# Kernel optimization log

Hardware: AMD Instinct MI355X
Metric: run time of the kernel (lower is better)

The kernel has to match this reference:

```python
import jax, jax.numpy as jnp
import numpy as np

BS, N, D, B, D_PM = 8, 4096, 1024, 8, 64
BUDGET = 16.0


def setup_inputs() -> dict:
    key = jax.random.key(0)
    ks = jax.random.split(key, 6)
    H = jax.random.normal(ks[0], (BS, N, D), jnp.float32)
    surprise = jax.random.normal(ks[1], (BS, N, D), jnp.float32)
    # W_pm initialized as (1/B)*I + small noise, as in initialize()
    eye = jnp.eye(D_PM, dtype=jnp.float32)
    W_pm = eye / B + 0.01 * jax.random.normal(ks[2], (BS, B, D_PM, D_PM), jnp.float32)
    proj_in_w = jax.random.normal(ks[3], (D_PM, D), jnp.float32) / np.float32(np.sqrt(D))
    proj_in_b = jnp.zeros((D_PM,), jnp.float32)
    # original zero-inits proj_out; use small values so output is non-trivial
    proj_out_w = 0.02 * jax.random.normal(ks[4], (D, D_PM), jnp.float32)
    proj_out_b = jnp.zeros((D,), jnp.float32)
    raw_beta = jnp.full((B,), -3.0, jnp.float32)
    raw_decay = jnp.full((B,), np.float32(np.log(0.999 / 0.001)), jnp.float32)  # logit(0.999)
    surp_scale = jnp.ones((1,), jnp.float32)
    surp_bias = jnp.zeros((1,), jnp.float32)
    return dict(H=H, surprise=surprise, W_pm=W_pm,
                proj_in_w=proj_in_w, proj_in_b=proj_in_b,
                proj_out_w=proj_out_w, proj_out_b=proj_out_b,
                raw_beta=raw_beta, raw_decay=raw_decay,
                surp_scale=surp_scale, surp_bias=surp_bias)


def reference(H, surprise, W_pm, proj_in_w, proj_in_b, proj_out_w, proj_out_b,
              raw_beta, raw_decay, surp_scale, surp_bias):
    # ---- read ----
    pre = jnp.einsum('bnd,pd->bnp', H, proj_in_w) + proj_in_b          # [BS,N,D_pm]
    W_sum = jnp.sum(W_pm, axis=1)                                      # [BS,D_pm,D_pm]
    post = jnp.einsum('bnp,bqp->bnq', pre, W_sum)                      # pre @ W_sum^T
    pm_read = jnp.einsum('bnq,dq->bnd', post, proj_out_w) + proj_out_b # [BS,N,D]
    # ---- commit (Hebbian, surprise-gated) ----
    surp_mag = jnp.linalg.norm(surprise, axis=-1)                      # [BS,N]
    s = jax.nn.sigmoid(surp_scale * surp_mag + surp_bias)              # [BS,N]
    weighted = jnp.sqrt(s)[..., None] * pre                            # [BS,N,D_pm]
    G = jnp.einsum('bnp,bnq->bpq', weighted, weighted) / N             # [BS,D_pm,D_pm]
    beta = jax.nn.softplus(raw_beta)                                   # [B]
    decay = jax.nn.sigmoid(raw_decay)                                  # [B]
    eye = jnp.eye(D_PM, dtype=pre.dtype)
    T = decay[None, :, None, None] * eye + beta[None, :, None, None] * G[:, None]  # [BS,B,D_pm,D_pm]
    W_new = jnp.einsum('bkij,bkjq->bkiq', W_pm, T)                     # [BS,B,D_pm,D_pm]
    frob = jnp.sqrt(jnp.sum(W_new * W_new, axis=(-2, -1), keepdims=True))
    scale = jnp.minimum(BUDGET / jnp.maximum(frob, 1e-8), 1.0)
    W_new = W_new * scale
    return pm_read, W_new
```

## Files before the change

kernel.cpp:

```cpp
#include <hip/hip_runtime.h>

typedef unsigned short u16;
typedef __attribute__((ext_vector_type(4))) float f32x4;
typedef __attribute__((ext_vector_type(8))) short s16x8;

static constexpr int N_ = 4096;
static constexpr int D_ = 1024;

__device__ __forceinline__ u16 f2bf(float f) {
  unsigned u = __float_as_uint(f);
  u += 0x7FFFu + ((u >> 16) & 1u);
  return (u16)(u >> 16);
}

__device__ __forceinline__ f32x4 zero4() {
  f32x4 z; z[0] = 0.f; z[1] = 0.f; z[2] = 0.f; z[3] = 0.f; return z;
}

__global__ __launch_bounds__(256) void k_prep(
    const float* __restrict__ Wpm, const float* __restrict__ piw,
    const float* __restrict__ pw, u16* __restrict__ WpB,
    u16* __restrict__ MB) {
  int bid = blockIdx.x, tid = threadIdx.x;
  if (bid < 16) {
    size_t i0 = (size_t)bid * 4096;
    for (int idx = tid; idx < 4096; idx += 256)
      WpB[i0 + idx] = f2bf(piw[i0 + idx]);
    return;
  }
  __shared__ float Ws[64][65];
  int idx2 = bid - 16;
  int b = idx2 >> 4, t = idx2 & 15;
  for (int idx = tid; idx < 4096; idx += 256) {
    float s = 0.f;
#pragma unroll
    for (int k = 0; k < 8; ++k)
      s += Wpm[((size_t)(b * 8 + k)) * 4096 + idx];
    Ws[idx >> 6][idx & 63] = s;
  }
  __syncthreads();
  u16* mb = MB + ((size_t)b << 16);
  for (int oidx = tid; oidx < 4096; oidx += 256) {
    int r = oidx >> 6, c = oidx & 63;
    int drow = t * 64 + r;
    const float* prow = pw + (size_t)drow * 64;
    float acc = 0.f;
#pragma unroll 8
    for (int q = 0; q < 64; ++q) acc += prow[q] * Ws[q][c];
    mb[(size_t)drow * 64 + c] = f2bf(acc);
  }
}

__global__ __launch_bounds__(512, 4) void k_main(
    const float* __restrict__ H, const float* __restrict__ Sur,
    const float* __restrict__ pib, const float* __restrict__ pob,
    const float* __restrict__ sscale_p, const float* __restrict__ sbias_p,
    const u16* __restrict__ WpB, const u16* __restrict__ MB,
    float* __restrict__ Gacc, float* __restrict__ out) {
  __shared__ float preF[64][68];
  __shared__ u16 preRP[64][72];
  __shared__ u16 wRP[64][72];
  __shared__ float sqs[64];

  const int tid = threadIdx.x;
  const int lane = tid & 63;
  const int w = tid >> 6;
  const int wm = w & 3;
  const int wk = w >> 2;
  const int llo = lane & 15;
  const int lhi = lane >> 4;
  const int b = blockIdx.x >> 6;
  const int row0 = (blockIdx.x & 63) * 64;

  {
    int r = w * 8 + (lane >> 3);
    const float* p = Sur + ((size_t)b * N_ + row0 + r) * D_ + (lane & 7) * 4;
    float a0 = 0.f, a1 = 0.f;
#pragma unroll 8
    for (int j = 0; j < 32; j += 2) {
      float4 v = *(const float4*)(p + j * 32);
      float4 v2 = *(const float4*)(p + j * 32 + 32);
      a0 += v.x * v.x + v.y * v.y + v.z * v.z + v.w * v.w;
      a1 += v2.x * v2.x + v2.y * v2.y + v2.z * v2.z + v2.w * v2.w;
    }
    float a = a0 + a1;
    a += __shfl_xor(a, 1, 64);
    a += __shfl_xor(a, 2, 64);
    a += __shfl_xor(a, 4, 64);
    if ((lane & 7) == 0) {
      float mag = sqrtf(a);
      float s = 1.f / (1.f + __expf(-(sscale_p[0] * mag + sbias_p[0])));
      sqs[r] = sqrtf(s);
    }
  }

  f32x4 accA[4];
#pragma unroll
  for (int t = 0; t < 4; ++t) accA[t] = zero4();
  {
    const float* hrow =
        H + ((size_t)b * N_ + row0 + wm * 16 + llo) * D_ + wk * 512 + lhi * 8;
    const u16* wp0 = WpB + (size_t)llo * 1024 + wk * 512 + lhi * 8;
#pragma unroll 2
    for (int k0 = 0; k0 < 512; k0 += 32) {
      float4 a0 = *(const float4*)(hrow + k0);
      float4 a1 = *(const float4*)(hrow + k0 + 4);
      s16x8 af;
      af[0] = (short)f2bf(a0.x); af[1] = (short)f2bf(a0.y);
      af[2] = (short)f2bf(a0.z); af[3] = (short)f2bf(a0.w);
      af[4] = (short)f2bf(a1.x); af[5] = (short)f2bf(a1.y);
      af[6] = (short)f2bf(a1.z); af[7] = (short)f2bf(a1.w);
#pragma unroll
      for (int t = 0; t < 4; ++t) {
        s16x8 bf = *(const s16x8*)(wp0 + (size_t)t * 16 * 1024 + k0);
        accA[t] = __builtin_amdgcn_mfma_f32_16x16x32_bf16(af, bf, accA[t], 0, 0, 0);
      }
    }
  }
  if (wk == 1) {
#pragma unroll
    for (int t = 0; t < 4; ++t)
#pragma unroll
      for (int r = 0; r < 4; ++r)
        preF[wm * 16 + lhi * 4 + r][t * 16 + llo] = accA[t][r];
  }
  __syncthreads();
  if (wk == 0) {
#pragma unroll
    for (int t = 0; t < 4; ++t) {
      float bias = pib[t * 16 + llo];
#pragma unroll
      for (int r = 0; r < 4; ++r) {
        int row = wm * 16 + lhi * 4 + r;
        float v = accA[t][r] + preF[row][t * 16 + llo] + bias;
        preRP[row][t * 16 + llo] = f2bf(v);
        wRP[row][t * 16 + llo] = f2bf(v * sqs[row]);
      }
    }
  }
  __syncthreads();

  {
    f32x4 accG[4];
#pragma unroll
    for (int t = 0; t < 4; ++t) accG[t] = zero4();
    int kbase = wk * 32;
    s16x8 ag;
#pragma unroll
    for (int j = 0; j < 8; ++j)
      ag[j] = (short)wRP[kbase + lhi * 8 + j][wm * 16 + llo];
#pragma unroll
    for (int t = 0; t < 4; ++t) {
      s16x8 bg;
#pragma unroll
      for (int j = 0; j < 8; ++j)
        bg[j] = (short)wRP[kbase + lhi * 8 + j][t * 16 + llo];
      accG[t] = __builtin_amdgcn_mfma_f32_16x16x32_bf16(ag, bg, accG[t], 0, 0, 0);
    }
    float* gb = Gacc + (size_t)b * 4096;
#pragma unroll
    for (int t = 0; t < 4; ++t)
#pragma unroll
      for (int r = 0; r < 4; ++r)
        atomicAdd(gb + (wm * 16 + lhi * 4 + r) * 64 + t * 16 + llo, accG[t][r]);
  }

  {
    s16x8 ad0 = *(const s16x8*)&preRP[wm * 16 + llo][lhi * 8];
    s16x8 ad1 = *(const s16x8*)&preRP[wm * 16 + llo][32 + lhi * 8];
    const u16* mb = MB + ((size_t)b << 16);
    float* orow = out + ((size_t)b * N_ + row0 + wm * 16) * D_;
    int nend = wk * 512 + 512;
    for (int n0 = wk * 512; n0 < nend; n0 += 16) {
      s16x8 b0 = *(const s16x8*)(mb + (size_t)(n0 + llo) * 64 + lhi * 8);
      s16x8 b1 = *(const s16x8*)(mb + (size_t)(n0 + llo) * 64 + 32 + lhi * 8);
      f32x4 acc = zero4();
      acc = __builtin_amdgcn_mfma_f32_16x16x32_bf16(ad0, b0, acc, 0, 0, 0);
      acc = __builtin_amdgcn_mfma_f32_16x16x32_bf16(ad1, b1, acc, 0, 0, 0);
      float bias = pob[n0 + llo];
#pragma unroll
      for (int r = 0; r < 4; ++r)
        orow[(size_t)(lhi * 4 + r) * D_ + n0 + llo] = acc[r] + bias;
    }
  }
}

__global__ __launch_bounds__(256) void k_wnew(
    const float* __restrict__ Wpm, const float* __restrict__ Gacc,
    const float* __restrict__ rbeta, const float* __restrict__ rdecay,
    float* __restrict__ outW) {
  __shared__ float Wk[64][66];
  __shared__ float Gl[64][66];
  __shared__ float red[4];
  int bk = blockIdx.x;
  int b = bk >> 3, k = bk & 7;
  int tid = threadIdx.x;
  const float* wsrc = Wpm + (size_t)bk * 4096;
  const float* gsrc = Gacc + (size_t)b * 4096;
  for (int idx = tid; idx < 4096; idx += 256) {
    Wk[idx >> 6][idx & 63] = wsrc[idx];
    Gl[idx >> 6][idx & 63] = gsrc[idx];
  }
  __syncthreads();
  float beta = log1pf(__expf(rbeta[k]));
  float decay = 1.f / (1.f + __expf(-rdecay[k]));
  float bn = beta * (1.f / 4096.f);
  int q = tid & 63;
  int rbase = tid >> 6;
  float vals[16];
  float ss = 0.f;
#pragma unroll
  for (int i = 0; i < 16; ++i) {
    int row = i * 4 + rbase;
    float acc = 0.f;
#pragma unroll 8
    for (int j = 0; j < 64; ++j) acc += Wk[row][j] * Gl[j][q];
    float v = decay * Wk[row][q] + bn * acc;
    vals[i] = v;
    ss += v * v;
  }
#pragma unroll
  for (int m = 1; m < 64; m <<= 1) ss += __shfl_xor(ss, m, 64);
  if ((tid & 63) == 0) red[tid >> 6] = ss;
  __syncthreads();
  float frob = sqrtf(red[0] + red[1] + red[2] + red[3]);
  float scale = fminf(16.f / fmaxf(frob, 1e-8f), 1.f);
  float* dst = outW + (size_t)bk * 4096;
#pragma unroll
  for (int i = 0; i < 16; ++i) dst[i * 256 + tid] = vals[i] * scale;
}

extern "C" void kernel_launch(void* const* d_in, const int* in_sizes, int n_in,
                              void* d_out, int out_size, void* d_ws, size_t ws_size,
                              hipStream_t stream) {
  const float* H      = (const float*)d_in[0];
  const float* Sur    = (const float*)d_in[1];
  const float* Wpm    = (const float*)d_in[2];
  const float* piw    = (const float*)d_in[3];
  const float* pib    = (const float*)d_in[4];
  const float* pw     = (const float*)d_in[5];
  const float* pob    = (const float*)d_in[6];
  const float* rbeta  = (const float*)d_in[7];
  const float* rdecay = (const float*)d_in[8];
  const float* sscale = (const float*)d_in[9];
  const float* sbias  = (const float*)d_in[10];
  float* out = (float*)d_out;

  char* ws = (char*)d_ws;
  float* Gacc = (float*)(ws);
  u16* WpB    = (u16*)(ws + 131072);
  u16* MB     = (u16*)(ws + 262144);

  hipMemsetAsync(Gacc, 0, 131072, stream);
  k_prep<<<144, 256, 0, stream>>>(Wpm, piw, pw, WpB, MB);
  k_main<<<512, 512, 0, stream>>>(H, Sur, pib, pob, sscale, sbias,
                                  WpB, MB, Gacc, out);
  k_wnew<<<64, 256, 0, stream>>>(Wpm, Gacc, rbeta, rdecay,
                                 out + (size_t)8 * 4096 * 1024);
}
```

Baseline: 165.6 us.

## Prefetch H and MB loads in registers, transpose wRP, fold Gacc zeroing

Software-pipelines the H loads in the projection GEMM with a 4-deep register buffer, and the MB loads in the output GEMM with a 2-deep buffer, so global latency overlaps with MFMA work. The weighted-pre tile is stored transposed in shared memory, so the Gram MFMA operands become single vector LDS reads instead of eight scalar gathers. Zeroing of the G accumulator moves into the prep kernel, which removes a separate memset launch. The cost is higher register pressure, which may reduce occupancy under the 512-thread launch bound.

```diff
diff --git a/kernel.cpp b/kernel.cpp
--- a/kernel.cpp
+++ b/kernel.cpp
@@ -20,12 +20,14 @@
 __global__ __launch_bounds__(256) void k_prep(
     const float* __restrict__ Wpm, const float* __restrict__ piw,
     const float* __restrict__ pw, u16* __restrict__ WpB,
-    u16* __restrict__ MB) {
+    u16* __restrict__ MB, float* __restrict__ Gacc) {
   int bid = blockIdx.x, tid = threadIdx.x;
   if (bid < 16) {
     size_t i0 = (size_t)bid * 4096;
     for (int idx = tid; idx < 4096; idx += 256)
       WpB[i0 + idx] = f2bf(piw[i0 + idx]);
+    float* g = Gacc + (size_t)bid * 2048;
+    for (int idx = tid; idx < 2048; idx += 256) g[idx] = 0.f;
     return;
   }
   __shared__ float Ws[64][65];
@@ -57,9 +59,9 @@
     const float* __restrict__ sscale_p, const float* __restrict__ sbias_p,
     const u16* __restrict__ WpB, const u16* __restrict__ MB,
     float* __restrict__ Gacc, float* __restrict__ out) {
-  __shared__ float preF[64][68];
-  __shared__ u16 preRP[64][72];
-  __shared__ u16 wRP[64][72];
+  __shared__ __align__(16) float preF[64][68];
+  __shared__ __align__(16) u16 preRP[64][72];
+  __shared__ __align__(16) u16 wRPT[64][72];
   __shared__ float sqs[64];
 
   const int tid = threadIdx.x;
@@ -76,7 +78,7 @@
     int r = w * 8 + (lane >> 3);
     const float* p = Sur + ((size_t)b * N_ + row0 + r) * D_ + (lane & 7) * 4;
     float a0 = 0.f, a1 = 0.f;
-#pragma unroll 8
+#pragma unroll
     for (int j = 0; j < 32; j += 2) {
       float4 v = *(const float4*)(p + j * 32);
       float4 v2 = *(const float4*)(p + j * 32 + 32);
@@ -101,19 +103,32 @@
     const float* hrow =
         H + ((size_t)b * N_ + row0 + wm * 16 + llo) * D_ + wk * 512 + lhi * 8;
     const u16* wp0 = WpB + (size_t)llo * 1024 + wk * 512 + lhi * 8;
-#pragma unroll 2
-    for (int k0 = 0; k0 < 512; k0 += 32) {
-      float4 a0 = *(const float4*)(hrow + k0);
-      float4 a1 = *(const float4*)(hrow + k0 + 4);
-      s16x8 af;
-      af[0] = (short)f2bf(a0.x); af[1] = (short)f2bf(a0.y);
-      af[2] = (short)f2bf(a0.z); af[3] = (short)f2bf(a0.w);
-      af[4] = (short)f2bf(a1.x); af[5] = (short)f2bf(a1.y);
-      af[6] = (short)f2bf(a1.z); af[7] = (short)f2bf(a1.w);
-#pragma unroll
-      for (int t = 0; t < 4; ++t) {
-        s16x8 bf = *(const s16x8*)(wp0 + (size_t)t * 16 * 1024 + k0);
-        accA[t] = __builtin_amdgcn_mfma_f32_16x16x32_bf16(af, bf, accA[t], 0, 0, 0);
+    float4 A0[4], A1[4];
+#pragma unroll
+    for (int i = 0; i < 4; ++i) {
+      A0[i] = *(const float4*)(hrow + i * 32);
+      A1[i] = *(const float4*)(hrow + i * 32 + 4);
+    }
+#pragma unroll
+    for (int kb = 0; kb < 512; kb += 128) {
+#pragma unroll
+      for (int jj = 0; jj < 4; ++jj) {
+        const int k0 = kb + jj * 32;
+        float4 a0 = A0[jj], a1 = A1[jj];
+        if (k0 + 128 < 512) {
+          A0[jj] = *(const float4*)(hrow + k0 + 128);
+          A1[jj] = *(const float4*)(hrow + k0 + 132);
+        }
+        s16x8 af;
+        af[0] = (short)f2bf(a0.x); af[1] = (short)f2bf(a0.y);
+        af[2] = (short)f2bf(a0.z); af[3] = (short)f2bf(a0.w);
+        af[4] = (short)f2bf(a1.x); af[5] = (short)f2bf(a1.y);
+        af[6] = (short)f2bf(a1.z); af[7] = (short)f2bf(a1.w);
+#pragma unroll
+        for (int t = 0; t < 4; ++t) {
+          s16x8 bf = *(const s16x8*)(wp0 + (size_t)t * 16384 + k0);
+          accA[t] = __builtin_amdgcn_mfma_f32_16x16x32_bf16(af, bf, accA[t], 0, 0, 0);
+        }
       }
     }
   }
@@ -134,27 +149,21 @@
         int row = wm * 16 + lhi * 4 + r;
         float v = accA[t][r] + preF[row][t * 16 + llo] + bias;
         preRP[row][t * 16 + llo] = f2bf(v);
-        wRP[row][t * 16 + llo] = f2bf(v * sqs[row]);
+        wRPT[t * 16 + llo][row] = f2bf(v * sqs[row]);
       }
     }
   }
   __syncthreads();
 
   {
+    const int kbase = wk * 32;
     f32x4 accG[4];
 #pragma unroll
     for (int t = 0; t < 4; ++t) accG[t] = zero4();
-    int kbase = wk * 32;
-    s16x8 ag;
-#pragma unroll
-    for (int j = 0; j < 8; ++j)
-      ag[j] = (short)wRP[kbase + lhi * 8 + j][wm * 16 + llo];
+    s16x8 ag = *(const s16x8*)&wRPT[wm * 16 + llo][kbase + lhi * 8];
 #pragma unroll
     for (int t = 0; t < 4; ++t) {
-      s16x8 bg;
-#pragma unroll
-      for (int j = 0; j < 8; ++j)
-        bg[j] = (short)wRP[kbase + lhi * 8 + j][t * 16 + llo];
+      s16x8 bg = *(const s16x8*)&wRPT[t * 16 + llo][kbase + lhi * 8];
       accG[t] = __builtin_amdgcn_mfma_f32_16x16x32_bf16(ag, bg, accG[t], 0, 0, 0);
     }
     float* gb = Gacc + (size_t)b * 4096;
@@ -169,14 +178,25 @@
     s16x8 ad0 = *(const s16x8*)&preRP[wm * 16 + llo][lhi * 8];
     s16x8 ad1 = *(const s16x8*)&preRP[wm * 16 + llo][32 + lhi * 8];
     const u16* mb = MB + ((size_t)b << 16);
+    const int nb = wk * 512;
+    const u16* mrow0 = mb + (size_t)(nb + llo) * 64 + lhi * 8;
     float* orow = out + ((size_t)b * N_ + row0 + wm * 16) * D_;
-    int nend = wk * 512 + 512;
-    for (int n0 = wk * 512; n0 < nend; n0 += 16) {
-      s16x8 b0 = *(const s16x8*)(mb + (size_t)(n0 + llo) * 64 + lhi * 8);
-      s16x8 b1 = *(const s16x8*)(mb + (size_t)(n0 + llo) * 64 + 32 + lhi * 8);
+    s16x8 B0[2], B1[2];
+    B0[0] = *(const s16x8*)(mrow0);
+    B1[0] = *(const s16x8*)(mrow0 + 32);
+    B0[1] = *(const s16x8*)(mrow0 + 1024);
+    B1[1] = *(const s16x8*)(mrow0 + 1024 + 32);
+#pragma unroll 2
+    for (int i = 0; i < 32; ++i) {
+      const int j = i & 1;
+      s16x8 b0 = B0[j], b1 = B1[j];
+      int ipf = (i + 2 < 32) ? (i + 2) : i;
+      B0[j] = *(const s16x8*)(mrow0 + (size_t)ipf * 1024);
+      B1[j] = *(const s16x8*)(mrow0 + (size_t)ipf * 1024 + 32);
       f32x4 acc = zero4();
       acc = __builtin_amdgcn_mfma_f32_16x16x32_bf16(ad0, b0, acc, 0, 0, 0);
       acc = __builtin_amdgcn_mfma_f32_16x16x32_bf16(ad1, b1, acc, 0, 0, 0);
+      const int n0 = nb + i * 16;
       float bias = pob[n0 + llo];
 #pragma unroll
       for (int r = 0; r < 4; ++r)
@@ -251,8 +271,7 @@
   u16* WpB    = (u16*)(ws + 131072);
   u16* MB     = (u16*)(ws + 262144);
 
-  hipMemsetAsync(Gacc, 0, 131072, stream);
-  k_prep<<<144, 256, 0, stream>>>(Wpm, piw, pw, WpB, MB);
+  k_prep<<<144, 256, 0, stream>>>(Wpm, piw, pw, WpB, MB, Gacc);
   k_main<<<512, 512, 0, stream>>>(H, Sur, pib, pob, sscale, sbias,
                                   WpB, MB, Gacc, out);
   k_wnew<<<64, 256, 0, stream>>>(Wpm, Gacc, rbeta, rdecay,
```

Result: no change. 168.1 us (+1.5%).

## Split fused main kernel into projection, read/Gram, and Gram-reduce stages

Applied to the files above, without the earlier changes.

Splits the single fused kernel into three. k1 uses small 16-row blocks: it computes the surprise gates and the input projection with a split-K over 4 waves, batching loads up front. k23 sums the four bf16 partial projections, builds the Gram tile and the output read with vectorized float4 stores. Per-block Gram partials are written in bf16 and reduced by k_gred, replacing the global float atomics and the memset. This adds bf16 round-trips through global memory for the projection partials and Gram partials, which costs extra traffic, two more launches and some precision.

```diff
diff --git a/kernel.cpp b/kernel.cpp
--- a/kernel.cpp
+++ b/kernel.cpp
@@ -1,26 +1,33 @@
 #include <hip/hip_runtime.h>
 
 typedef unsigned short u16;
+typedef unsigned int u32;
 typedef __attribute__((ext_vector_type(4))) float f32x4;
 typedef __attribute__((ext_vector_type(8))) short s16x8;
+typedef __attribute__((ext_vector_type(4))) short s16x4;
 
 static constexpr int N_ = 4096;
 static constexpr int D_ = 1024;
+
+#define MEMCLOB() asm volatile("" ::: "memory")
 
 __device__ __forceinline__ u16 f2bf(float f) {
   unsigned u = __float_as_uint(f);
   u += 0x7FFFu + ((u >> 16) & 1u);
   return (u16)(u >> 16);
 }
-
+__device__ __forceinline__ float bf2f(u16 v) {
+  return __uint_as_float((u32)v << 16);
+}
 __device__ __forceinline__ f32x4 zero4() {
   f32x4 z; z[0] = 0.f; z[1] = 0.f; z[2] = 0.f; z[3] = 0.f; return z;
 }
 
-__global__ __launch_bounds__(256) void k_prep(
+__global__ __launch_bounds__(256) void k_aux(
     const float* __restrict__ Wpm, const float* __restrict__ piw,
     const float* __restrict__ pw, u16* __restrict__ WpB,
     u16* __restrict__ MB) {
+  __shared__ float Ws[64][65];
   int bid = blockIdx.x, tid = threadIdx.x;
   if (bid < 16) {
     size_t i0 = (size_t)bid * 4096;
@@ -28,7 +35,6 @@
       WpB[i0 + idx] = f2bf(piw[i0 + idx]);
     return;
   }
-  __shared__ float Ws[64][65];
   int idx2 = bid - 16;
   int b = idx2 >> 4, t = idx2 & 15;
   for (int idx = tid; idx < 4096; idx += 256) {
@@ -51,17 +57,85 @@
   }
 }
 
-__global__ __launch_bounds__(512, 4) void k_main(
+__global__ __launch_bounds__(256, 4) void k1(
     const float* __restrict__ H, const float* __restrict__ Sur,
-    const float* __restrict__ pib, const float* __restrict__ pob,
     const float* __restrict__ sscale_p, const float* __restrict__ sbias_p,
-    const u16* __restrict__ WpB, const u16* __restrict__ MB,
-    float* __restrict__ Gacc, float* __restrict__ out) {
-  __shared__ float preF[64][68];
-  __shared__ u16 preRP[64][72];
-  __shared__ u16 wRP[64][72];
-  __shared__ float sqs[64];
-
+    const u16* __restrict__ WpB, u16* __restrict__ preQ,
+    float* __restrict__ sqs_ws) {
+  const int tid = threadIdx.x;
+  const int lane = tid & 63;
+  const int w = tid >> 6;
+  const int llo = lane & 15;
+  const int lhi = lane >> 4;
+  const int b = blockIdx.x >> 8;
+  const int row0 = (blockIdx.x & 255) * 16;
+
+  {
+    const float* sp =
+        Sur + ((size_t)b * N_ + row0 + (tid >> 4)) * D_ + (tid & 15) * 4;
+    float4 sv[16];
+#pragma unroll
+    for (int i = 0; i < 16; ++i) sv[i] = *(const float4*)(sp + i * 64);
+    MEMCLOB();
+    float a = 0.f;
+#pragma unroll
+    for (int i = 0; i < 16; ++i)
+      a += sv[i].x * sv[i].x + sv[i].y * sv[i].y + sv[i].z * sv[i].z +
+           sv[i].w * sv[i].w;
+    a += __shfl_xor(a, 1, 64);
+    a += __shfl_xor(a, 2, 64);
+    a += __shfl_xor(a, 4, 64);
+    a += __shfl_xor(a, 8, 64);
+    if ((tid & 15) == 0) {
+      float mag = sqrtf(a);
+      float s = 1.f / (1.f + __expf(-(sscale_p[0] * mag + sbias_p[0])));
+      sqs_ws[b * N_ + row0 + (tid >> 4)] = sqrtf(s);
+    }
+  }
+
+  const float* hrow =
+      H + ((size_t)b * N_ + row0 + llo) * D_ + w * 256 + lhi * 8;
+  float4 ah[16];
+#pragma unroll
+  for (int c = 0; c < 8; ++c) {
+    ah[2 * c] = *(const float4*)(hrow + c * 32);
+    ah[2 * c + 1] = *(const float4*)(hrow + c * 32 + 4);
+  }
+  MEMCLOB();
+  f32x4 acc[4];
+#pragma unroll
+  for (int t = 0; t < 4; ++t) acc[t] = zero4();
+  const u16* wpb = WpB + w * 256 + lhi * 8;
+#pragma unroll
+  for (int c = 0; c < 8; ++c) {
+    s16x8 af;
+    af[0] = (short)f2bf(ah[2 * c].x); af[1] = (short)f2bf(ah[2 * c].y);
+    af[2] = (short)f2bf(ah[2 * c].z); af[3] = (short)f2bf(ah[2 * c].w);
+    af[4] = (short)f2bf(ah[2 * c + 1].x); af[5] = (short)f2bf(ah[2 * c + 1].y);
+    af[6] = (short)f2bf(ah[2 * c + 1].z); af[7] = (short)f2bf(ah[2 * c + 1].w);
+#pragma unroll
+    for (int t = 0; t < 4; ++t) {
+      s16x8 bs = *(const s16x8*)(wpb + (size_t)(t * 16 + llo) * 1024 + c * 32);
+      acc[t] = __builtin_amdgcn_mfma_f32_16x16x32_bf16(bs, af, acc[t], 0, 0, 0);
+    }
+  }
+  u16* pq = preQ + ((size_t)w << 21) + ((size_t)(b * N_ + row0 + llo)) * 64;
+#pragma unroll
+  for (int t = 0; t < 4; ++t) {
+    s16x4 v;
+#pragma unroll
+    for (int r = 0; r < 4; ++r) v[r] = (short)f2bf(acc[t][r]);
+    *(s16x4*)(pq + t * 16 + lhi * 4) = v;
+  }
+}
+
+__global__ __launch_bounds__(512, 4) void k23(
+    const u16* __restrict__ preQ, const float* __restrict__ pib,
+    const float* __restrict__ pob, const u16* __restrict__ MB,
+    const float* __restrict__ sqs_ws, u16* __restrict__ GpartB,
+    float* __restrict__ out) {
+  __shared__ __align__(16) u16 preRP[64 * 80];
+  __shared__ __align__(16) u16 wRPT[64 * 80];
   const int tid = threadIdx.x;
   const int lane = tid & 63;
   const int w = tid >> 6;
@@ -73,120 +147,97 @@
   const int row0 = (blockIdx.x & 63) * 64;
 
   {
-    int r = w * 8 + (lane >> 3);
-    const float* p = Sur + ((size_t)b * N_ + row0 + r) * D_ + (lane & 7) * 4;
-    float a0 = 0.f, a1 = 0.f;
+    const int row = tid >> 3, col0 = (tid & 7) * 8;
+    const u16* pq = preQ + ((size_t)(b * N_ + row0 + row)) * 64 + col0;
+    float sum[8] = {0, 0, 0, 0, 0, 0, 0, 0};
+#pragma unroll
+    for (int q = 0; q < 4; ++q) {
+      s16x8 v = *(const s16x8*)(pq + (size_t)q * 2097152);
+#pragma unroll
+      for (int j = 0; j < 8; ++j) sum[j] += bf2f((u16)v[j]);
+    }
+    float4 bb0 = *(const float4*)&pib[col0];
+    float4 bb1 = *(const float4*)&pib[col0 + 4];
+    sum[0] += bb0.x; sum[1] += bb0.y; sum[2] += bb0.z; sum[3] += bb0.w;
+    sum[4] += bb1.x; sum[5] += bb1.y; sum[6] += bb1.z; sum[7] += bb1.w;
+    float sq = sqs_ws[b * N_ + row0 + row];
+    s16x8 pr;
+#pragma unroll
+    for (int j = 0; j < 8; ++j) pr[j] = (short)f2bf(sum[j]);
+    *(s16x8*)&preRP[row * 80 + col0] = pr;
+#pragma unroll
+    for (int j = 0; j < 8; ++j)
+      wRPT[(col0 + j) * 80 + row] = f2bf(sum[j] * sq);
+  }
+  __syncthreads();
+
+  {
+    s16x8 ag = *(const s16x8*)&wRPT[(wm * 16 + llo) * 80 + wk * 32 + lhi * 8];
+    f32x4 accG[4];
+#pragma unroll
+    for (int t = 0; t < 4; ++t) {
+      s16x8 bg = *(const s16x8*)&wRPT[(t * 16 + llo) * 80 + wk * 32 + lhi * 8];
+      accG[t] = __builtin_amdgcn_mfma_f32_16x16x32_bf16(ag, bg, zero4(), 0, 0, 0);
+    }
+    u16* gout = GpartB + ((size_t)blockIdx.x * 2 + wk) * 4096;
+#pragma unroll
+    for (int t = 0; t < 4; ++t)
+#pragma unroll
+      for (int r = 0; r < 4; ++r)
+        gout[(wm * 16 + lhi * 4 + r) * 64 + t * 16 + llo] = f2bf(accG[t][r]);
+  }
+
+  {
+    s16x8 ad0 = *(const s16x8*)&preRP[(wm * 16 + llo) * 80 + lhi * 8];
+    s16x8 ad1 = *(const s16x8*)&preRP[(wm * 16 + llo) * 80 + 32 + lhi * 8];
+    const u16* mcol = MB + ((size_t)b << 16) + (size_t)(wk * 512) * 64 + lhi * 8;
+    float* orow = out + ((size_t)b * N_ + row0 + wm * 16 + llo) * D_ + wk * 512;
+    const float* pobw = pob + wk * 512;
+#pragma unroll
+    for (int c = 0; c < 8; ++c) {
+      s16x8 f0[4], f1[4];
+#pragma unroll
+      for (int i = 0; i < 4; ++i) {
+        const u16* p = mcol + (size_t)(c * 64 + i * 16 + llo) * 64;
+        f0[i] = *(const s16x8*)p;
+        f1[i] = *(const s16x8*)(p + 32);
+      }
+#pragma unroll
+      for (int i = 0; i < 4; ++i) {
+        f32x4 acc = zero4();
+        acc = __builtin_amdgcn_mfma_f32_16x16x32_bf16(f0[i], ad0, acc, 0, 0, 0);
+        acc = __builtin_amdgcn_mfma_f32_16x16x32_bf16(f1[i], ad1, acc, 0, 0, 0);
+        int n0 = c * 64 + i * 16 + lhi * 4;
+        float4 bias4 = *(const float4*)&pobw[n0];
+        float4 o;
+        o.x = acc[0] + bias4.x;
+        o.y = acc[1] + bias4.y;
+        o.z = acc[2] + bias4.z;
+        o.w = acc[3] + bias4.w;
+        *(float4*)(orow + n0) = o;
+      }
+    }
+  }
+}
+
+__global__ __launch_bounds__(256) void k_gred(
+    const u16* __restrict__ GpartB, float* __restrict__ Gsum) {
+  __shared__ float red[4][64];
+  int b = blockIdx.x >> 6, g = blockIdx.x & 63;
+  int lane = threadIdx.x & 63, q = threadIdx.x >> 6;
+  const u16* src = GpartB + ((size_t)(b * 128 + q * 32)) * 4096 + g * 64 + lane;
+  float s = 0.f;
 #pragma unroll 8
-    for (int j = 0; j < 32; j += 2) {
-      float4 v = *(const float4*)(p + j * 32);
-      float4 v2 = *(const float4*)(p + j * 32 + 32);
-      a0 += v.x * v.x + v.y * v.y + v.z * v.z + v.w * v.w;
-      a1 += v2.x * v2.x + v2.y * v2.y + v2.z * v2.z + v2.w * v2.w;
-    }
-    float a = a0 + a1;
-    a += __shfl_xor(a, 1, 64);
-    a += __shfl_xor(a, 2, 64);
-    a += __shfl_xor(a, 4, 64);
-    if ((lane & 7) == 0) {
-      float mag = sqrtf(a);
-      float s = 1.f / (1.f + __expf(-(sscale_p[0] * mag + sbias_p[0])));
-      sqs[r] = sqrtf(s);
-    }
-  }
-
-  f32x4 accA[4];
-#pragma unroll
-  for (int t = 0; t < 4; ++t) accA[t] = zero4();
-  {
-    const float* hrow =
-        H + ((size_t)b * N_ + row0 + wm * 16 + llo) * D_ + wk * 512 + lhi * 8;
-    const u16* wp0 = WpB + (size_t)llo * 1024 + wk * 512 + lhi * 8;
-#pragma unroll 2
-    for (int k0 = 0; k0 < 512; k0 += 32) {
-      float4 a0 = *(const float4*)(hrow + k0);
-      float4 a1 = *(const float4*)(hrow + k0 + 4);
-      s16x8 af;
-      af[0] = (short)f2bf(a0.x); af[1] = (short)f2bf(a0.y);
-      af[2] = (short)f2bf(a0.z); af[3] = (short)f2bf(a0.w);
-      af[4] = (short)f2bf(a1.x); af[5] = (short)f2bf(a1.y);
-      af[6] = (short)f2bf(a1.z); af[7] = (short)f2bf(a1.w);
-#pragma unroll
-      for (int t = 0; t < 4; ++t) {
-        s16x8 bf = *(const s16x8*)(wp0 + (size_t)t * 16 * 1024 + k0);
-        accA[t] = __builtin_amdgcn_mfma_f32_16x16x32_bf16(af, bf, accA[t], 0, 0, 0);
-      }
-    }
-  }
-  if (wk == 1) {
-#pragma unroll
-    for (int t = 0; t < 4; ++t)
-#pragma unroll
-      for (int r = 0; r < 4; ++r)
-        preF[wm * 16 + lhi * 4 + r][t * 16 + llo] = accA[t][r];
-  }
-  __syncthreads();
-  if (wk == 0) {
-#pragma unroll
-    for (int t = 0; t < 4; ++t) {
-      float bias = pib[t * 16 + llo];
-#pragma unroll
-      for (int r = 0; r < 4; ++r) {
-        int row = wm * 16 + lhi * 4 + r;
-        float v = accA[t][r] + preF[row][t * 16 + llo] + bias;
-        preRP[row][t * 16 + llo] = f2bf(v);
-        wRP[row][t * 16 + llo] = f2bf(v * sqs[row]);
-      }
-    }
-  }
-  __syncthreads();
-
-  {
-    f32x4 accG[4];
-#pragma unroll
-    for (int t = 0; t < 4; ++t) accG[t] = zero4();
-    int kbase = wk * 32;
-    s16x8 ag;
-#pragma unroll
-    for (int j = 0; j < 8; ++j)
-      ag[j] = (short)wRP[kbase + lhi * 8 + j][wm * 16 + llo];
-#pragma unroll
-    for (int t = 0; t < 4; ++t) {
-      s16x8 bg;
-#pragma unroll
-      for (int j = 0; j < 8; ++j)
-        bg[j] = (short)wRP[kbase + lhi * 8 + j][t * 16 + llo];
-      accG[t] = __builtin_amdgcn_mfma_f32_16x16x32_bf16(ag, bg, accG[t], 0, 0, 0);
-    }
-    float* gb = Gacc + (size_t)b * 4096;
-#pragma unroll
-    for (int t = 0; t < 4; ++t)
-#pragma unroll
-      for (int r = 0; r < 4; ++r)
-        atomicAdd(gb + (wm * 16 + lhi * 4 + r) * 64 + t * 16 + llo, accG[t][r]);
-  }
-
-  {
-    s16x8 ad0 = *(const s16x8*)&preRP[wm * 16 + llo][lhi * 8];
-    s16x8 ad1 = *(const s16x8*)&preRP[wm * 16 + llo][32 + lhi * 8];
-    const u16* mb = MB + ((size_t)b << 16);
-    float* orow = out + ((size_t)b * N_ + row0 + wm * 16) * D_;
-    int nend = wk * 512 + 512;
-    for (int n0 = wk * 512; n0 < nend; n0 += 16) {
-      s16x8 b0 = *(const s16x8*)(mb + (size_t)(n0 + llo) * 64 + lhi * 8);
-      s16x8 b1 = *(const s16x8*)(mb + (size_t)(n0 + llo) * 64 + 32 + lhi * 8);
-      f32x4 acc = zero4();
-      acc = __builtin_amdgcn_mfma_f32_16x16x32_bf16(ad0, b0, acc, 0, 0, 0);
-      acc = __builtin_amdgcn_mfma_f32_16x16x32_bf16(ad1, b1, acc, 0, 0, 0);
-      float bias = pob[n0 + llo];
-#pragma unroll
-      for (int r = 0; r < 4; ++r)
-        orow[(size_t)(lhi * 4 + r) * D_ + n0 + llo] = acc[r] + bias;
-    }
-  }
+  for (int i = 0; i < 32; ++i) s += bf2f(src[(size_t)i * 4096]);
+  red[q][lane] = s;
+  __syncthreads();
+  if (q == 0)
+    Gsum[(size_t)b * 4096 + g * 64 + lane] =
+        red[0][lane] + red[1][lane] + red[2][lane] + red[3][lane];
 }
 
 __global__ __launch_bounds__(256) void k_wnew(
-    const float* __restrict__ Wpm, const float* __restrict__ Gacc,
+    const float* __restrict__ Wpm, const float* __restrict__ Gsum,
     const float* __restrict__ rbeta, const float* __restrict__ rdecay,
     float* __restrict__ outW) {
   __shared__ float Wk[64][66];
@@ -196,7 +247,7 @@
   int b = bk >> 3, k = bk & 7;
   int tid = threadIdx.x;
   const float* wsrc = Wpm + (size_t)bk * 4096;
-  const float* gsrc = Gacc + (size_t)b * 4096;
+  const float* gsrc = Gsum + (size_t)b * 4096;
   for (int idx = tid; idx < 4096; idx += 256) {
     Wk[idx >> 6][idx & 63] = wsrc[idx];
     Gl[idx >> 6][idx & 63] = gsrc[idx];
@@ -247,14 +298,17 @@
   float* out = (float*)d_out;
 
   char* ws = (char*)d_ws;
-  float* Gacc = (float*)(ws);
-  u16* WpB    = (u16*)(ws + 131072);
-  u16* MB     = (u16*)(ws + 262144);
-
-  hipMemsetAsync(Gacc, 0, 131072, stream);
-  k_prep<<<144, 256, 0, stream>>>(Wpm, piw, pw, WpB, MB);
-  k_main<<<512, 512, 0, stream>>>(H, Sur, pib, pob, sscale, sbias,
-                                  WpB, MB, Gacc, out);
-  k_wnew<<<64, 256, 0, stream>>>(Wpm, Gacc, rbeta, rdecay,
+  u16* WpB      = (u16*)(ws);
+  u16* MB       = (u16*)(ws + 131072);
+  float* sqs_ws = (float*)(ws + 1179648);
+  float* Gsum   = (float*)(ws + 1310720);
+  u16* GpartB   = (u16*)(ws + 1441792);
+  u16* preQ     = (u16*)(ws + 9830400);
+
+  k_aux<<<144, 256, 0, stream>>>(Wpm, piw, pw, WpB, MB);
+  k1<<<2048, 256, 0, stream>>>(H, Sur, sscale, sbias, WpB, preQ, sqs_ws);
+  k23<<<512, 512, 0, stream>>>(preQ, pib, pob, MB, sqs_ws, GpartB, out);
+  k_gred<<<512, 256, 0, stream>>>(GpartB, Gsum);
+  k_wnew<<<64, 256, 0, stream>>>(Wpm, Gsum, rbeta, rdecay,
                                  out + (size_t)8 * 4096 * 1024);
 }
```

Measured after the change: 181.7 us. 9.7% more time.
